# Performance work log

Measured on AMD Instinct MI355X. Metric: run time of the kernel, lower is better.

## Reference

```python
import jax, jax.numpy as jnp
import numpy as np

WINDOW_SIZE = 128

def setup_inputs() -> dict:
    key = jax.random.key(0)
    kq, kk, kv = jax.random.split(key, 3)
    B, S, D = 4, 4096, 128
    q = jax.random.normal(kq, (B, S, D), dtype=jnp.float32)
    k = jax.random.normal(kk, (B, S, D), dtype=jnp.float32)
    v = jax.random.normal(kv, (B, S, D), dtype=jnp.float32)
    return {"q": q, "k": k, "v": v}

def reference(q, k, v):
    B, S, D = q.shape
    q = q / jnp.sqrt(jnp.asarray(D, q.dtype))
    # band mask: tril(window_size-1) & triu(-(window_size-1)) == |i - j| <= window_size-1
    i = jax.lax.broadcasted_iota(jnp.int32, (S, S), 0)
    j = jax.lax.broadcasted_iota(jnp.int32, (S, S), 1)
    mask = jnp.abs(i - j) <= (WINDOW_SIZE - 1)
    scores = jnp.einsum('bqd,bkd->bqk', q, k)  # [B,S,S]
    scores = jnp.where(mask, scores, jnp.asarray(-1e9, scores.dtype))
    weights = jax.nn.softmax(scores, axis=-1)
    return jnp.einsum('bqk,bkd->bqd', weights, v)
```

## Files before the change

### kernel.cpp

```cpp
#include <hip/hip_runtime.h>


typedef __attribute__((ext_vector_type(8))) _Float16 half8;
typedef __attribute__((ext_vector_type(2))) __fp16 fp16x2;
typedef __attribute__((ext_vector_type(4))) float floatx4;

#define MFMA_F16(a, b, c) __builtin_amdgcn_mfma_f32_16x16x32_f16(a, b, c, 0, 0, 0)

constexpr int S_ = 4096, D_ = 128, W_ = 127;
constexpr int BQ = 32, BK = 64;
constexpr int KST = 136;
constexpr int PST = 36;
constexpr int OST = 132;

union SMem {
  struct {
    _Float16 Kh[2][BK * KST];
    _Float16 Vt[2][D_ * 64];
    _Float16 Ps[4][16 * PST];
  } a;
  struct {
    float Om[4][16 * OST];
    float l_[4][16];
  } b;
};

__device__ __forceinline__ unsigned pk2(float a, float b) {
  union { fp16x2 h; unsigned u; } cvt;
  cvt.h = __builtin_amdgcn_cvt_pkrtz(a, b);
  return cvt.u;
}

__global__ __launch_bounds__(256, 2)
void swa_v3_kernel(const float* __restrict__ qg, const float* __restrict__ kg,
                   const float* __restrict__ vg, float* __restrict__ og)
{
  __shared__ __align__(16) SMem sm;
  const int tid  = threadIdx.x;
  const int lane = tid & 63;
  const int wave = tid >> 6;
  const int lx   = lane & 15;
  const int quad = lane >> 4;
  const int wq   = wave >> 1;
  const int par  = wave & 1;

  const int qtiles = S_ / BQ;
  const int bb = blockIdx.x / qtiles;
  const int q0 = (blockIdx.x % qtiles) * BQ;

  const float* qb = qg + (size_t)bb * S_ * D_;
  const float* kb = kg + (size_t)bb * S_ * D_;
  const float* vb = vg + (size_t)bb * S_ * D_;
  float*       ob = og + (size_t)bb * S_ * D_;

  const int qrow = q0 + 16 * wq + lx;
  half8 qh[4], ql[4];
#pragma unroll
  for (int ks = 0; ks < 4; ++ks) {
    const float* p = qb + (size_t)qrow * D_ + 32 * ks + 8 * quad;
#pragma unroll
    for (int j = 0; j < 8; ++j) {
      float f = p[j];
      _Float16 h = (_Float16)f;
      qh[ks][j] = h;
      ql[ks][j] = (_Float16)(f - (float)h);
    }
  }

  floatx4 o[8];
#pragma unroll
  for (int dt = 0; dt < 8; ++dt) o[dt] = (floatx4){0.f, 0.f, 0.f, 0.f};
  float lp[4] = {0.f, 0.f, 0.f, 0.f};

  const int kstart = (q0 > W_) ? (q0 - W_) : 0;
  int kend = q0 + BQ - 1 + W_;
  if (kend > S_ - 1) kend = S_ - 1;
  const int c0 = kstart >> 6, c1 = kend >> 6;

  const int ilo = q0 + 16 * wq, ihi = ilo + 15;
  const float C1 = 0.12751727f, C2 = -5.7707802f;

  const int kr16 = tid >> 4, c8 = tid & 15;
  const int r0 = tid >> 5, c4v = tid & 31;

  float4 kf[8], vf[8];
#pragma unroll
  for (int j = 0; j < 4; ++j) {
    const float* src = kb + (size_t)(c0 * BK + kr16 + 16 * j) * D_ + 8 * c8;
    kf[2 * j]     = *(const float4*)(src);
    kf[2 * j + 1] = *(const float4*)(src + 4);
  }
#pragma unroll
  for (int u = 0; u < 8; ++u)
    vf[u] = *(const float4*)(vb + (size_t)(c0 * BK + 8 * r0 + u) * D_ + 4 * c4v);

  for (int c = c0; c <= c1; ++c) {
    const int buf = c & 1;
#pragma unroll
    for (int j = 0; j < 4; ++j) {
      const float* f0 = (const float*)&kf[2 * j];
      const float* f1 = (const float*)&kf[2 * j + 1];
      uint4 kh8;
      kh8.x = pk2(f0[0], f0[1]);
      kh8.y = pk2(f0[2], f0[3]);
      kh8.z = pk2(f1[0], f1[1]);
      kh8.w = pk2(f1[2], f1[3]);
      *(uint4*)(&sm.a.Kh[buf][(kr16 + 16 * j) * KST + 8 * c8]) = kh8;
    }
#pragma unroll
    for (int i = 0; i < 4; ++i) {
      uint4 tv;
      tv.x = pk2(((const float*)&vf[0])[i], ((const float*)&vf[1])[i]);
      tv.y = pk2(((const float*)&vf[2])[i], ((const float*)&vf[3])[i]);
      tv.z = pk2(((const float*)&vf[4])[i], ((const float*)&vf[5])[i]);
      tv.w = pk2(((const float*)&vf[6])[i], ((const float*)&vf[7])[i]);
      const int g = r0 ^ (c4v & 7);
      *(uint4*)(&sm.a.Vt[buf][(4 * c4v + i) * 64 + 8 * g]) = tv;
    }
    __syncthreads();
    if (c < c1) {
#pragma unroll
      for (int j = 0; j < 4; ++j) {
        const float* src = kb + (size_t)((c + 1) * BK + kr16 + 16 * j) * D_ + 8 * c8;
        kf[2 * j]     = *(const float4*)(src);
        kf[2 * j + 1] = *(const float4*)(src + 4);
      }
#pragma unroll
      for (int u = 0; u < 8; ++u)
        vf[u] = *(const float4*)(vb + (size_t)((c + 1) * BK + 8 * r0 + u) * D_ + 4 * c4v);
    }

    const int kcp = c * BK + 32 * par;
    if (kcp + 31 < ilo - W_ || kcp > ihi + W_) continue;

    floatx4 acc0 = {0.f, 0.f, 0.f, 0.f}, acc1 = {0.f, 0.f, 0.f, 0.f};
#pragma unroll
    for (int ks = 0; ks < 4; ++ks) {
      const int dof = 32 * ks + 8 * quad;
      half8 b0 = *(const half8*)(&sm.a.Kh[buf][(32 * par + lx) * KST + dof]);
      half8 b1 = *(const half8*)(&sm.a.Kh[buf][(32 * par + 16 + lx) * KST + dof]);
      acc0 = MFMA_F16(qh[ks], b0, acc0);
      acc1 = MFMA_F16(qh[ks], b1, acc1);
      acc0 = MFMA_F16(ql[ks], b0, acc0);
      acc1 = MFMA_F16(ql[ks], b1, acc1);
    }

    const int ibase = q0 + 16 * wq + 4 * quad;
#pragma unroll
    for (int r = 0; r < 4; ++r) {
      const int i = ibase + r;
      const bool v0 = (unsigned)(kcp + lx - i + W_)      <= (unsigned)(2 * W_);
      const bool v1 = (unsigned)(kcp + 16 + lx - i + W_) <= (unsigned)(2 * W_);
      const float e0 = __builtin_amdgcn_exp2f(__builtin_fmaf(acc0[r], C1, C2));
      const float e1 = __builtin_amdgcn_exp2f(__builtin_fmaf(acc1[r], C1, C2));
      const float p0 = v0 ? e0 : 0.f;
      const float p1 = v1 ? e1 : 0.f;
      lp[r] += p0 + p1;
      sm.a.Ps[wave][(4 * quad + r) * PST + lx]      = (_Float16)p0;
      sm.a.Ps[wave][(4 * quad + r) * PST + 16 + lx] = (_Float16)p1;
    }
    asm volatile("s_waitcnt lgkmcnt(0)" ::: "memory");
    half8 pa = *(const half8*)(&sm.a.Ps[wave][lx * PST + 8 * quad]);

#pragma unroll
    for (int dt = 0; dt < 8; ++dt) {
      const int d = 16 * dt + lx;
      const int g = (4 * par + quad) ^ ((d >> 2) & 7);
      half8 vfr = *(const half8*)(&sm.a.Vt[buf][d * 64 + 8 * g]);
      o[dt] = MFMA_F16(pa, vfr, o[dt]);
    }
  }

#pragma unroll
  for (int r = 0; r < 4; ++r) {
    float s = lp[r];
    s += __shfl_xor(s, 1);
    s += __shfl_xor(s, 2);
    s += __shfl_xor(s, 4);
    s += __shfl_xor(s, 8);
    lp[r] = s;
  }

  __syncthreads();
#pragma unroll
  for (int dt = 0; dt < 8; ++dt)
#pragma unroll
    for (int r = 0; r < 4; ++r)
      sm.b.Om[wave][(4 * quad + r) * OST + 16 * dt + lx] = o[dt][r];
  if (lx == 0) {
#pragma unroll
    for (int r = 0; r < 4; ++r) sm.b.l_[wave][4 * quad + r] = lp[r];
  }
  __syncthreads();

  const int row32 = tid >> 3, cc8 = tid & 7;
  const int g2 = row32 >> 4, r16 = row32 & 15;
  const float inv = 1.f / (sm.b.l_[2 * g2][r16] + sm.b.l_[2 * g2 + 1][r16]);
  const float* Oa = &sm.b.Om[2 * g2][r16 * OST + 16 * cc8];
  const float* Ob = &sm.b.Om[2 * g2 + 1][r16 * OST + 16 * cc8];
  float* dst = ob + (size_t)(q0 + row32) * D_ + 16 * cc8;
#pragma unroll
  for (int t = 0; t < 4; ++t) {
    float4 xa = *(const float4*)(Oa + 4 * t);
    float4 xb = *(const float4*)(Ob + 4 * t);
    float4 r4;
    r4.x = (xa.x + xb.x) * inv;
    r4.y = (xa.y + xb.y) * inv;
    r4.z = (xa.z + xb.z) * inv;
    r4.w = (xa.w + xb.w) * inv;
    *(float4*)(dst + 4 * t) = r4;
  }
}

extern "C" void kernel_launch(void* const* d_in, const int* in_sizes, int n_in,
                              void* d_out, int out_size, void* d_ws, size_t ws_size,
                              hipStream_t stream) {
  const float* q = (const float*)d_in[0];
  const float* k = (const float*)d_in[1];
  const float* v = (const float*)d_in[2];
  float* out = (float*)d_out;

  const int B = in_sizes[0] / (S_ * D_);
  dim3 grid(B * (S_ / BQ));
  dim3 block(256);
  swa_v3_kernel<<<grid, block, 0, stream>>>(q, k, v, out);
}
```

Baseline: 97.38 us.

## Split key chunks across 8 waves with single-buffered LDS and K/V loader halves

Doubles the block to 512 threads (8 waves). Four waves per 16-row query group rotate over 32-key sub-chunks, so more waves share each K/V tile. The K/V staging is single-buffered, with one half of the threads loading K and the other half loading V. Block IDs are remapped to interleave tiles, which may help spread work across XCDs or improve L2 locality. The aim is more latency hiding and more concurrent MFMA work per block, at the cost of an extra barrier per chunk, idle waves on alternate chunks, and a 4-way partial-sum reduction in the epilogue.

```diff
diff --git a/kernel.cpp b/kernel.cpp
--- a/kernel.cpp
+++ b/kernel.cpp
@@ -15,13 +15,13 @@
 
 union SMem {
   struct {
-    _Float16 Kh[2][BK * KST];
-    _Float16 Vt[2][D_ * 64];
-    _Float16 Ps[4][16 * PST];
+    _Float16 Kh[BK * KST];
+    _Float16 Vt[D_ * 64];
+    _Float16 Ps[8][16 * PST];
   } a;
   struct {
-    float Om[4][16 * OST];
-    float l_[4][16];
+    float Om[8][16 * OST];
+    float l_[8][16];
   } b;
 };
 
@@ -31,8 +31,8 @@
   return cvt.u;
 }
 
-__global__ __launch_bounds__(256, 2)
-void swa_v3_kernel(const float* __restrict__ qg, const float* __restrict__ kg,
+__global__ __launch_bounds__(512, 4)
+void swa_v4_kernel(const float* __restrict__ qg, const float* __restrict__ kg,
                    const float* __restrict__ vg, float* __restrict__ og)
 {
   __shared__ __align__(16) SMem sm;
@@ -41,12 +41,13 @@
   const int wave = tid >> 6;
   const int lx   = lane & 15;
   const int quad = lane >> 4;
-  const int wq   = wave >> 1;
-  const int par  = wave & 1;
-
-  const int qtiles = S_ / BQ;
-  const int bb = blockIdx.x / qtiles;
-  const int q0 = (blockIdx.x % qtiles) * BQ;
+  const int wq   = wave >> 2;
+  const int par  = wave & 3;
+
+  const int bid = blockIdx.x;
+  const int lid = (bid & 7) * 64 + (bid >> 3);
+  const int bb  = lid >> 7;
+  const int q0  = (lid & 127) * BQ;
 
   const float* qb = qg + (size_t)bb * S_ * D_;
   const float* kb = kg + (size_t)bb * S_ * D_;
@@ -80,65 +81,79 @@
   const int ilo = q0 + 16 * wq, ihi = ilo + 15;
   const float C1 = 0.12751727f, C2 = -5.7707802f;
 
+  const int sh   = tid >> 8;
   const int kr16 = tid >> 4, c8 = tid & 15;
-  const int r0 = tid >> 5, c4v = tid & 31;
-
-  float4 kf[8], vf[8];
-#pragma unroll
-  for (int j = 0; j < 4; ++j) {
-    const float* src = kb + (size_t)(c0 * BK + kr16 + 16 * j) * D_ + 8 * c8;
-    kf[2 * j]     = *(const float4*)(src);
-    kf[2 * j + 1] = *(const float4*)(src + 4);
-  }
-#pragma unroll
-  for (int u = 0; u < 8; ++u)
-    vf[u] = *(const float4*)(vb + (size_t)(c0 * BK + 8 * r0 + u) * D_ + 4 * c4v);
+  const int t2   = tid & 255;
+  const int r0   = t2 >> 5, c4v = t2 & 31;
+
+  float4 pf[8];
+  if (sh == 0) {
+#pragma unroll
+    for (int j = 0; j < 4; ++j) {
+      const float* src = kb + (size_t)(c0 * BK + kr16 + 16 * j) * D_ + 8 * c8;
+      pf[2 * j]     = *(const float4*)(src);
+      pf[2 * j + 1] = *(const float4*)(src + 4);
+    }
+  } else {
+#pragma unroll
+    for (int u = 0; u < 8; ++u)
+      pf[u] = *(const float4*)(vb + (size_t)(c0 * BK + 8 * r0 + u) * D_ + 4 * c4v);
+  }
 
   for (int c = c0; c <= c1; ++c) {
-    const int buf = c & 1;
-#pragma unroll
-    for (int j = 0; j < 4; ++j) {
-      const float* f0 = (const float*)&kf[2 * j];
-      const float* f1 = (const float*)&kf[2 * j + 1];
-      uint4 kh8;
-      kh8.x = pk2(f0[0], f0[1]);
-      kh8.y = pk2(f0[2], f0[3]);
-      kh8.z = pk2(f1[0], f1[1]);
-      kh8.w = pk2(f1[2], f1[3]);
-      *(uint4*)(&sm.a.Kh[buf][(kr16 + 16 * j) * KST + 8 * c8]) = kh8;
-    }
-#pragma unroll
-    for (int i = 0; i < 4; ++i) {
-      uint4 tv;
-      tv.x = pk2(((const float*)&vf[0])[i], ((const float*)&vf[1])[i]);
-      tv.y = pk2(((const float*)&vf[2])[i], ((const float*)&vf[3])[i]);
-      tv.z = pk2(((const float*)&vf[4])[i], ((const float*)&vf[5])[i]);
-      tv.w = pk2(((const float*)&vf[6])[i], ((const float*)&vf[7])[i]);
-      const int g = r0 ^ (c4v & 7);
-      *(uint4*)(&sm.a.Vt[buf][(4 * c4v + i) * 64 + 8 * g]) = tv;
+    __syncthreads();
+    if (sh == 0) {
+#pragma unroll
+      for (int j = 0; j < 4; ++j) {
+        const float* f0 = (const float*)&pf[2 * j];
+        const float* f1 = (const float*)&pf[2 * j + 1];
+        uint4 kh8;
+        kh8.x = pk2(f0[0], f0[1]);
+        kh8.y = pk2(f0[2], f0[3]);
+        kh8.z = pk2(f1[0], f1[1]);
+        kh8.w = pk2(f1[2], f1[3]);
+        *(uint4*)(&sm.a.Kh[(kr16 + 16 * j) * KST + 8 * c8]) = kh8;
+      }
+    } else {
+#pragma unroll
+      for (int i = 0; i < 4; ++i) {
+        uint4 tv;
+        tv.x = pk2(((const float*)&pf[0])[i], ((const float*)&pf[1])[i]);
+        tv.y = pk2(((const float*)&pf[2])[i], ((const float*)&pf[3])[i]);
+        tv.z = pk2(((const float*)&pf[4])[i], ((const float*)&pf[5])[i]);
+        tv.w = pk2(((const float*)&pf[6])[i], ((const float*)&pf[7])[i]);
+        const int g = r0 ^ (c4v & 7);
+        *(uint4*)(&sm.a.Vt[(4 * c4v + i) * 64 + 8 * g]) = tv;
+      }
     }
     __syncthreads();
     if (c < c1) {
-#pragma unroll
-      for (int j = 0; j < 4; ++j) {
-        const float* src = kb + (size_t)((c + 1) * BK + kr16 + 16 * j) * D_ + 8 * c8;
-        kf[2 * j]     = *(const float4*)(src);
-        kf[2 * j + 1] = *(const float4*)(src + 4);
+      if (sh == 0) {
+#pragma unroll
+        for (int j = 0; j < 4; ++j) {
+          const float* src = kb + (size_t)((c + 1) * BK + kr16 + 16 * j) * D_ + 8 * c8;
+          pf[2 * j]     = *(const float4*)(src);
+          pf[2 * j + 1] = *(const float4*)(src + 4);
+        }
+      } else {
+#pragma unroll
+        for (int u = 0; u < 8; ++u)
+          pf[u] = *(const float4*)(vb + (size_t)((c + 1) * BK + 8 * r0 + u) * D_ + 4 * c4v);
       }
-#pragma unroll
-      for (int u = 0; u < 8; ++u)
-        vf[u] = *(const float4*)(vb + (size_t)((c + 1) * BK + 8 * r0 + u) * D_ + 4 * c4v);
-    }
-
-    const int kcp = c * BK + 32 * par;
+    }
+
+    const int sb = 2 * (c - c0);
+    const int h  = (par - sb) & 3;
+    if (h > 1) continue;
+    const int kcp = c * BK + 32 * h;
     if (kcp + 31 < ilo - W_ || kcp > ihi + W_) continue;
 
     floatx4 acc0 = {0.f, 0.f, 0.f, 0.f}, acc1 = {0.f, 0.f, 0.f, 0.f};
 #pragma unroll
     for (int ks = 0; ks < 4; ++ks) {
       const int dof = 32 * ks + 8 * quad;
-      half8 b0 = *(const half8*)(&sm.a.Kh[buf][(32 * par + lx) * KST + dof]);
-      half8 b1 = *(const half8*)(&sm.a.Kh[buf][(32 * par + 16 + lx) * KST + dof]);
+      half8 b0 = *(const half8*)(&sm.a.Kh[(32 * h + lx) * KST + dof]);
+      half8 b1 = *(const half8*)(&sm.a.Kh[(32 * h + 16 + lx) * KST + dof]);
       acc0 = MFMA_F16(qh[ks], b0, acc0);
       acc1 = MFMA_F16(qh[ks], b1, acc1);
       acc0 = MFMA_F16(ql[ks], b0, acc0);
@@ -165,8 +180,8 @@
 #pragma unroll
     for (int dt = 0; dt < 8; ++dt) {
       const int d = 16 * dt + lx;
-      const int g = (4 * par + quad) ^ ((d >> 2) & 7);
-      half8 vfr = *(const half8*)(&sm.a.Vt[buf][d * 64 + 8 * g]);
+      const int g = (4 * h + quad) ^ ((d >> 2) & 7);
+      half8 vfr = *(const half8*)(&sm.a.Vt[d * 64 + 8 * g]);
       o[dt] = MFMA_F16(pa, vfr, o[dt]);
     }
   }
@@ -193,22 +208,24 @@
   }
   __syncthreads();
 
-  const int row32 = tid >> 3, cc8 = tid & 7;
-  const int g2 = row32 >> 4, r16 = row32 & 15;
-  const float inv = 1.f / (sm.b.l_[2 * g2][r16] + sm.b.l_[2 * g2 + 1][r16]);
-  const float* Oa = &sm.b.Om[2 * g2][r16 * OST + 16 * cc8];
-  const float* Ob = &sm.b.Om[2 * g2 + 1][r16 * OST + 16 * cc8];
-  float* dst = ob + (size_t)(q0 + row32) * D_ + 16 * cc8;
-#pragma unroll
-  for (int t = 0; t < 4; ++t) {
-    float4 xa = *(const float4*)(Oa + 4 * t);
-    float4 xb = *(const float4*)(Ob + 4 * t);
-    float4 r4;
-    r4.x = (xa.x + xb.x) * inv;
-    r4.y = (xa.y + xb.y) * inv;
-    r4.z = (xa.z + xb.z) * inv;
-    r4.w = (xa.w + xb.w) * inv;
-    *(float4*)(dst + 4 * t) = r4;
+  const int row = tid >> 4, cd = tid & 15;
+  const int g2 = row >> 4, r16 = row & 15;
+  float lsum = 0.f;
+#pragma unroll
+  for (int p = 0; p < 4; ++p) lsum += sm.b.l_[4 * g2 + p][r16];
+  const float inv = 1.f / lsum;
+
+  float* dst = ob + (size_t)(q0 + row) * D_ + 8 * cd;
+#pragma unroll
+  for (int t = 0; t < 2; ++t) {
+    float4 acc = {0.f, 0.f, 0.f, 0.f};
+#pragma unroll
+    for (int p = 0; p < 4; ++p) {
+      float4 x = *(const float4*)(&sm.b.Om[4 * g2 + p][r16 * OST + 8 * cd + 4 * t]);
+      acc.x += x.x; acc.y += x.y; acc.z += x.z; acc.w += x.w;
+    }
+    acc.x *= inv; acc.y *= inv; acc.z *= inv; acc.w *= inv;
+    *(float4*)(dst + 4 * t) = acc;
   }
 }
 
@@ -222,6 +239,6 @@
 
   const int B = in_sizes[0] / (S_ * D_);
   dim3 grid(B * (S_ / BQ));
-  dim3 block(256);
-  swa_v3_kernel<<<grid, block, 0, stream>>>(q, k, v, out);
+  dim3 block(512);
+  swa_v4_kernel<<<grid, block, 0, stream>>>(q, k, v, out);
 }
```

Result: slower. 111.2 us (+14.2%).
